# Kernel optimization log

Hardware: AMD Instinct MI355X
Metric: run time of the kernel (lower is better)

## Reference

```python
import jax, jax.numpy as jnp
import numpy as np

EPS = 1e-5
AVG_D_LOG = 2.302585092994046  # avg_d['log'] = log(10)

N, D, F, FE = 65536, 16, 64, 16
POST_IN = (4 * 3 + 1) * F  # (n_agg*n_scalers + 1) * in_dim = 832


def setup_inputs() -> dict:
    key = jax.random.key(0)
    ks = jax.random.split(key, 8)
    h = jax.random.normal(ks[0], (N, F), dtype=jnp.float32)
    edge_attr = jax.random.normal(ks[1], (N, D, FE), dtype=jnp.float32)
    nbr_idx = jax.random.randint(ks[2], (N, D), 0, N)
    pre_in = 2 * F + FE
    W_pre = jax.random.normal(ks[3], (pre_in, F), dtype=jnp.float32) / np.sqrt(pre_in)
    b_pre = jnp.zeros((F,), dtype=jnp.float32)
    W_post1 = jax.random.normal(ks[4], (POST_IN, F), dtype=jnp.float32) / np.sqrt(POST_IN)
    b_post1 = jnp.zeros((F,), dtype=jnp.float32)
    W_post2 = jax.random.normal(ks[5], (F, F), dtype=jnp.float32) / np.sqrt(F)
    b_post2 = jnp.zeros((F,), dtype=jnp.float32)
    return {"h": h, "edge_attr": edge_attr, "nbr_idx": nbr_idx,
            "W_pre": W_pre, "b_pre": b_pre,
            "W_post1": W_post1, "b_post1": b_post1,
            "W_post2": W_post2, "b_post2": b_post2}


def reference(h, edge_attr, nbr_idx, W_pre, b_pre, W_post1, b_post1, W_post2, b_post2):
    # pretrans: message MLP on cat([src_feat, dst_feat, edge_attr])
    h_src = h[nbr_idx]                                   # [N, D, F]
    h_dst = jnp.broadcast_to(h[:, None, :], h_src.shape)  # [N, D, F]
    z = jnp.concatenate([h_src, h_dst, edge_attr], axis=-1)  # [N, D, 2F+FE]
    e = jax.nn.relu(jnp.einsum('ndi,io->ndo', z, W_pre) + b_pre)  # [N, D, F]

    # multi-aggregator neighbor reduction (dim=-2)
    mean = jnp.mean(e, axis=-2)
    mx = jnp.max(e, axis=-2)
    mn = jnp.min(e, axis=-2)
    var = jax.nn.relu(jnp.mean(e * e, axis=-2) - mean * mean)
    std = jnp.sqrt(var + EPS)
    agg = jnp.concatenate([mean, mx, mn, std], axis=-1)  # [N, 4F]

    # degree scalers (fixed in-degree D)
    logD = jnp.asarray(np.log(D + 1.0), dtype=h.dtype)
    amp = agg * (logD / AVG_D_LOG)
    att = agg * (AVG_D_LOG / logD)
    agg = jnp.concatenate([agg, amp, att], axis=-1)      # [N, 12F]

    # posttrans MLP on cat([h, aggregated]) with residual (in_dim == out_dim)
    x = jnp.concatenate([h, agg], axis=-1)               # [N, 13F]
    x = jax.nn.relu(x @ W_post1 + b_post1)
    x = x @ W_post2 + b_post2
    return x + h
```

## Files before the change

### kernel.cpp

```cpp
#include <hip/hip_runtime.h>
#include <hip/hip_bf16.h>
#include <math.h>


#define N_NODES 65536
#define NBLK (N_NODES / 16)
#define GRID_PREP (NBLK + 64)
#define ASTRIDE 348
#define YSTRIDE 76

typedef float f32x4 __attribute__((ext_vector_type(4)));
typedef float f32x16 __attribute__((ext_vector_type(16)));
typedef short s16x8 __attribute__((ext_vector_type(8)));
typedef unsigned short us4 __attribute__((ext_vector_type(4)));
typedef int i32x4 __attribute__((ext_vector_type(4)));

__device__ __forceinline__ unsigned short f2bf(float f) {
    union { float f; unsigned int u; } v; v.f = f;
    unsigned int r = v.u + 0x7fffu + ((v.u >> 16) & 1u);
    return (unsigned short)(r >> 16);
}
__device__ __forceinline__ unsigned short f2bfh(float f) {
    __hip_bfloat16 b = __float2bfloat16(f);
    union { __hip_bfloat16 b; unsigned short u; } v; v.b = b; return v.u;
}
__device__ __forceinline__ float bf2f(unsigned short u) {
    union { unsigned int u; float f; } v; v.u = ((unsigned int)u) << 16; return v.f;
}

__global__ __launch_bounds__(256) void k_prep(const float* __restrict__ h,
                                              const float* __restrict__ Wpre,
                                              const float* __restrict__ b_pre,
                                              const float* __restrict__ Wp1,
                                              const float* __restrict__ Wp2,
                                              unsigned short* __restrict__ u,
                                              unsigned short* __restrict__ vbf,
                                              unsigned short* __restrict__ wfullT,
                                              unsigned short* __restrict__ w3T,
                                              unsigned short* __restrict__ wp2T,
                                              float c1, float c2) {
    int t = threadIdx.x;
    if (blockIdx.x >= NBLK) {
        int c = blockIdx.x - NBLK;
        for (int k = t; k < 320; k += 256) {
            float v;
            if (k < 64) v = Wp1[k * 64 + c];
            else {
                int kk = k - 64;
                v = Wp1[(64 + kk) * 64 + c] + c1 * Wp1[(320 + kk) * 64 + c]
                                            + c2 * Wp1[(576 + kk) * 64 + c];
            }
            wfullT[c * 320 + k] = f2bf(v);
        }
        if (t < 16)              w3T[c * 16 + t]         = f2bf(Wpre[(128 + t) * 64 + c]);
        if (t >= 64 && t < 128)  wp2T[c * 64 + (t - 64)] = f2bf(Wp2[(t - 64) * 64 + c]);
        return;
    }

    __shared__ unsigned short hl[16 * 68];
    int lane = t & 63;
    int wv = __builtin_amdgcn_readfirstlane(t) >> 6;
    int c = lane & 15, g = lane >> 4;
    int node0 = blockIdx.x * 16;
    {
        int r = t >> 4, q = t & 15;
        float4 hv = *((const float4*)(h + (size_t)node0 * 64) + t);
        us4 o;
        o.x = f2bfh(hv.x); o.y = f2bfh(hv.y); o.z = f2bfh(hv.z); o.w = f2bfh(hv.w);
        *(us4*)&hl[r * 68 + q * 4] = o;
    }
    s16x8 bf[2][2];
    int woff = (wv < 2) ? 0 : 64;
    #pragma unroll
    for (int i2 = 0; i2 < 2; ++i2) {
        int wcol = ((wv & 1) * 32) + i2 * 16 + c;
        #pragma unroll
        for (int ks = 0; ks < 2; ++ks) {
            #pragma unroll
            for (int j = 0; j < 8; ++j)
                bf[i2][ks][j] = (short)f2bfh(Wpre[(woff + ks * 32 + g * 8 + j) * 64 + wcol]);
        }
    }
    __syncthreads();
    f32x4 acc0 = {0.f, 0.f, 0.f, 0.f}, acc1 = {0.f, 0.f, 0.f, 0.f};
    #pragma unroll
    for (int ks = 0; ks < 2; ++ks) {
        s16x8 a = *(const s16x8*)&hl[c * 68 + ks * 32 + g * 8];
        acc0 = __builtin_amdgcn_mfma_f32_16x16x32_bf16(a, bf[0][ks], acc0, 0, 0, 0);
        acc1 = __builtin_amdgcn_mfma_f32_16x16x32_bf16(a, bf[1][ks], acc1, 0, 0, 0);
    }
    unsigned short* dst = (wv < 2) ? u : vbf;
    #pragma unroll
    for (int i2 = 0; i2 < 2; ++i2) {
        int dcol = ((wv & 1) * 32) + i2 * 16 + c;
        float bp = (wv < 2) ? b_pre[dcol] : 0.f;
        const f32x4& av = i2 ? acc1 : acc0;
        #pragma unroll
        for (int i = 0; i < 4; ++i) {
            int row = g * 4 + i;
            dst[(size_t)(node0 + row) * 64 + dcol] = f2bfh(av[i] + bp);
        }
    }
}

__global__ __launch_bounds__(256, 4) void k_main(
    const float* __restrict__ h,
    const float* __restrict__ edge_attr,
    const int* __restrict__ nbr_idx,
    const float* __restrict__ b_post1,
    const float* __restrict__ b_post2,
    const unsigned short* __restrict__ u,
    const unsigned short* __restrict__ vbf,
    const unsigned short* __restrict__ wfullT,
    const unsigned short* __restrict__ w3T,
    const unsigned short* __restrict__ wp2T,
    float* __restrict__ out) {
    __shared__ unsigned short A_lds[16 * ASTRIDE];
    __shared__ unsigned short y1_lds[16 * YSTRIDE];

    int t = threadIdx.x;
    int lane = t & 63;
    int wu2 = __builtin_amdgcn_readfirstlane(t) >> 6;
    int c = lane & 15;
    int g = lane >> 4;
    int l32 = lane & 31;
    int h2 = lane >> 5;
    int ct = wu2 & 1;
    int wr = wu2 >> 1;
    int colb = ct * 32 + l32;
    int cb2 = colb * 2;
    int col16 = wu2 * 16 + c;
    int node0 = blockIdx.x * 16;

    s16x8 w3b = *(const s16x8*)&w3T[colb * 16 + h2 * 8];
    float b1c = b_post1[col16];
    float b2c = b_post2[col16];

    const char* ub = (const char*)u;
    const char* vb = (const char*)vbf + ((unsigned)node0 << 7) + (unsigned)(wr * 256) + cb2;
    const char* eb = (const char*)edge_attr
                   + ((size_t)node0 * 16 + wr * 32 + l32) * 64 + h2 * 32;

    {
        int r = t >> 4, q = t & 15;
        float4 hv = *((const float4*)(h + (size_t)node0 * 64) + t);
        us4 o;
        o.x = f2bfh(hv.x); o.y = f2bfh(hv.y); o.z = f2bfh(hv.z); o.w = f2bfh(hv.w);
        *(us4*)&A_lds[r * ASTRIDE + q * 4] = o;
    }

#define ISSUE(S, IT)                                                           \
    const int* nb##S = nbr_idx + node0 * 16 + (wr + 2 * (IT)) * 32 + 4 * h2;   \
    i32x4 ja##S = *(const i32x4*)(nb##S);                                      \
    i32x4 jb##S = *(const i32x4*)(nb##S + 8);                                  \
    i32x4 jc##S = *(const i32x4*)(nb##S + 16);                                 \
    i32x4 jd##S = *(const i32x4*)(nb##S + 24);                                 \
    float4 xa##S = *(const float4*)(eb + (IT) * 4096);                         \
    float4 xb##S = *(const float4*)(eb + (IT) * 4096 + 16);                    \
    unsigned short g0##S  = *(const unsigned short*)(ub + (unsigned)((ja##S[0] << 7) + cb2)); \
    unsigned short g1##S  = *(const unsigned short*)(ub + (unsigned)((ja##S[1] << 7) + cb2)); \
    unsigned short g2##S  = *(const unsigned short*)(ub + (unsigned)((ja##S[2] << 7) + cb2)); \
    unsigned short g3##S  = *(const unsigned short*)(ub + (unsigned)((ja##S[3] << 7) + cb2)); \
    unsigned short g4##S  = *(const unsigned short*)(ub + (unsigned)((jb##S[0] << 7) + cb2)); \
    unsigned short g5##S  = *(const unsigned short*)(ub + (unsigned)((jb##S[1] << 7) + cb2)); \
    unsigned short g6##S  = *(const unsigned short*)(ub + (unsigned)((jb##S[2] << 7) + cb2)); \
    unsigned short g7##S  = *(const unsigned short*)(ub + (unsigned)((jb##S[3] << 7) + cb2)); \
    unsigned short g8##S  = *(const unsigned short*)(ub + (unsigned)((jc##S[0] << 7) + cb2)); \
    unsigned short g9##S  = *(const unsigned short*)(ub + (unsigned)((jc##S[1] << 7) + cb2)); \
    unsigned short g10##S = *(const unsigned short*)(ub + (unsigned)((jc##S[2] << 7) + cb2)); \
    unsigned short g11##S = *(const unsigned short*)(ub + (unsigned)((jc##S[3] << 7) + cb2)); \
    unsigned short g12##S = *(const unsigned short*)(ub + (unsigned)((jd##S[0] << 7) + cb2)); \
    unsigned short g13##S = *(const unsigned short*)(ub + (unsigned)((jd##S[1] << 7) + cb2)); \
    unsigned short g14##S = *(const unsigned short*)(ub + (unsigned)((jd##S[2] << 7) + cb2)); \
    unsigned short g15##S = *(const unsigned short*)(ub + (unsigned)((jd##S[3] << 7) + cb2)); \
    unsigned short va##S = *(const unsigned short*)(vb + (IT) * 512);          \
    unsigned short vc##S = *(const unsigned short*)(vb + (IT) * 512 + 128);

#define COMPUTE(S, IT) {                                                       \
    s16x8 a;                                                                   \
    a[0] = (short)f2bfh(xa##S.x); a[1] = (short)f2bfh(xa##S.y);                \
    a[2] = (short)f2bfh(xa##S.z); a[3] = (short)f2bfh(xa##S.w);                \
    a[4] = (short)f2bfh(xb##S.x); a[5] = (short)f2bfh(xb##S.y);                \
    a[6] = (short)f2bfh(xb##S.z); a[7] = (short)f2bfh(xb##S.w);                \
    f32x16 acc = {};                                                           \
    acc = __builtin_amdgcn_mfma_f32_32x32x16_bf16(a, w3b, acc, 0, 0, 0);       \
    float v0 = bf2f(va##S), v1 = bf2f(vc##S);                                  \
    float e0  = fmaxf(acc[0]  + bf2f(g0##S)  + v0, 0.f);                       \
    float e1  = fmaxf(acc[1]  + bf2f(g1##S)  + v0, 0.f);                       \
    float e2  = fmaxf(acc[2]  + bf2f(g2##S)  + v0, 0.f);                       \
    float e3  = fmaxf(acc[3]  + bf2f(g3##S)  + v0, 0.f);                       \
    float e4  = fmaxf(acc[4]  + bf2f(g4##S)  + v0, 0.f);                       \
    float e5  = fmaxf(acc[5]  + bf2f(g5##S)  + v0, 0.f);                       \
    float e6  = fmaxf(acc[6]  + bf2f(g6##S)  + v0, 0.f);                       \
    float e7  = fmaxf(acc[7]  + bf2f(g7##S)  + v0, 0.f);                       \
    float e8  = fmaxf(acc[8]  + bf2f(g8##S)  + v1, 0.f);                       \
    float e9  = fmaxf(acc[9]  + bf2f(g9##S)  + v1, 0.f);                       \
    float e10 = fmaxf(acc[10] + bf2f(g10##S) + v1, 0.f);                       \
    float e11 = fmaxf(acc[11] + bf2f(g11##S) + v1, 0.f);                       \
    float e12 = fmaxf(acc[12] + bf2f(g12##S) + v1, 0.f);                       \
    float e13 = fmaxf(acc[13] + bf2f(g13##S) + v1, 0.f);                       \
    float e14 = fmaxf(acc[14] + bf2f(g14##S) + v1, 0.f);                       \
    float e15 = fmaxf(acc[15] + bf2f(g15##S) + v1, 0.f);                       \
    float s1a = ((e0 + e1) + (e2 + e3)) + ((e4 + e5) + (e6 + e7));             \
    float s2a = fmaf(e0, e0, fmaf(e1, e1, fmaf(e2, e2, e3 * e3)))              \
              + fmaf(e4, e4, fmaf(e5, e5, fmaf(e6, e6, e7 * e7)));             \
    float mxa = fmaxf(fmaxf(fmaxf(e0, e1), fmaxf(e2, e3)),                     \
                      fmaxf(fmaxf(e4, e5), fmaxf(e6, e7)));                    \
    float mna = fminf(fminf(fminf(e0, e1), fminf(e2, e3)),                     \
                      fminf(fminf(e4, e5), fminf(e6, e7)));                    \
    float s1b = ((e8 + e9) + (e10 + e11)) + ((e12 + e13) + (e14 + e15));       \
    float s2b = fmaf(e8, e8, fmaf(e9, e9, fmaf(e10, e10, e11 * e11)))          \
              + fmaf(e12, e12, fmaf(e13, e13, fmaf(e14, e14, e15 * e15)));     \
    float mxb = fmaxf(fmaxf(fmaxf(e8, e9), fmaxf(e10, e11)),                   \
                      fmaxf(fmaxf(e12, e13), fmaxf(e14, e15)));                \
    float mnb = fminf(fminf(fminf(e8, e9), fminf(e10, e11)),                   \
                      fminf(fminf(e12, e13), fminf(e14, e15)));                \
    s1a += __shfl_xor(s1a, 32); s2a += __shfl_xor(s2a, 32);                    \
    mxa = fmaxf(mxa, __shfl_xor(mxa, 32)); mna = fminf(mna, __shfl_xor(mna, 32)); \
    s1b += __shfl_xor(s1b, 32); s2b += __shfl_xor(s2b, 32);                    \
    mxb = fmaxf(mxb, __shfl_xor(mxb, 32)); mnb = fminf(mnb, __shfl_xor(mnb, 32)); \
    float S1 = h2 ? s1b : s1a;                                                 \
    float S2 = h2 ? s2b : s2a;                                                 \
    float MX = h2 ? mxb : mxa;                                                 \
    float MN = h2 ? mnb : mna;                                                 \
    float M  = S1 * 0.0625f;                                                   \
    float SD = sqrtf(fmaxf(fmaf(-M, M, S2 * 0.0625f), 0.f) + 1e-5f);           \
    unsigned short* pd = &A_lds[(2 * (wr + 2 * (IT)) + h2) * ASTRIDE + 64 + colb]; \
    pd[0]   = f2bfh(M);                                                        \
    pd[64]  = f2bfh(MX);                                                       \
    pd[128] = f2bfh(MN);                                                       \
    pd[192] = f2bfh(SD);                                                       \
}

    ISSUE(T0, 0)
    ISSUE(T1, 1)
    COMPUTE(T0, 0)
    ISSUE(T2, 2)
    COMPUTE(T1, 1)
    ISSUE(T3, 3)
    COMPUTE(T2, 2)
    COMPUTE(T3, 3)
#undef ISSUE
#undef COMPUTE

    s16x8 wf[10];
    #pragma unroll
    for (int ks = 0; ks < 10; ++ks)
        wf[ks] = *(const s16x8*)&wfullT[col16 * 320 + ks * 32 + g * 8];
    __syncthreads();

    {
        f32x4 y1 = {0.f, 0.f, 0.f, 0.f};
        #pragma unroll
        for (int ks = 0; ks < 10; ++ks) {
            s16x8 a = *(const s16x8*)&A_lds[c * ASTRIDE + ks * 32 + g * 8];
            y1 = __builtin_amdgcn_mfma_f32_16x16x32_bf16(a, wf[ks], y1, 0, 0, 0);
        }
        #pragma unroll
        for (int i = 0; i < 4; ++i)
            y1_lds[(g * 4 + i) * YSTRIDE + col16] = f2bfh(fmaxf(y1[i] + b1c, 0.f));
    }

    s16x8 wp0 = *(const s16x8*)&wp2T[col16 * 64 + 0 * 32 + g * 8];
    s16x8 wp1 = *(const s16x8*)&wp2T[col16 * 64 + 1 * 32 + g * 8];
    __syncthreads();

    {
        f32x4 o = {0.f, 0.f, 0.f, 0.f};
        {
            s16x8 a0 = *(const s16x8*)&y1_lds[c * YSTRIDE + 0 * 32 + g * 8];
            s16x8 a1 = *(const s16x8*)&y1_lds[c * YSTRIDE + 1 * 32 + g * 8];
            o = __builtin_amdgcn_mfma_f32_16x16x32_bf16(a0, wp0, o, 0, 0, 0);
            o = __builtin_amdgcn_mfma_f32_16x16x32_bf16(a1, wp1, o, 0, 0, 0);
        }
        #pragma unroll
        for (int i = 0; i < 4; ++i) {
            int r = g * 4 + i;
            out[(size_t)(node0 + r) * 64 + col16] =
                o[i] + b2c + h[(size_t)(node0 + r) * 64 + col16];
        }
    }
}

extern "C" void kernel_launch(void* const* d_in, const int* in_sizes, int n_in,
                              void* d_out, int out_size, void* d_ws, size_t ws_size,
                              hipStream_t stream) {
    const float* h         = (const float*)d_in[0];
    const float* edge_attr = (const float*)d_in[1];
    const int*   nbr_idx   = (const int*)d_in[2];
    const float* W_pre     = (const float*)d_in[3];
    const float* b_pre     = (const float*)d_in[4];
    const float* W_post1   = (const float*)d_in[5];
    const float* b_post1   = (const float*)d_in[6];
    const float* W_post2   = (const float*)d_in[7];
    const float* b_post2   = (const float*)d_in[8];
    float* out = (float*)d_out;

    size_t need = (size_t)N_NODES * 64 * 2 * 2 + (64 * 320 + 64 * 16 + 64 * 64) * 2;
    if (ws_size < need) return;
    unsigned short* u      = (unsigned short*)d_ws;
    unsigned short* vbf    = u + (size_t)N_NODES * 64;
    unsigned short* wfullT = vbf + (size_t)N_NODES * 64;
    unsigned short* w3T    = wfullT + 64 * 320;
    unsigned short* wp2T   = w3T + 64 * 16;

    double ld = log(16.0 + 1.0);
    const double AVG = 2.302585092994046;
    float c1 = (float)(ld / AVG);
    float c2 = (float)(AVG / ld);

    k_prep<<<GRID_PREP, 256, 0, stream>>>(h, W_pre, b_pre, W_post1, W_post2,
                                          u, vbf, wfullT, w3T, wp2T, c1, c2);
    k_main<<<NBLK, 256, 0, stream>>>(h, edge_attr, nbr_idx, b_post1, b_post2,
                                     u, vbf, wfullT, w3T, wp2T, out);
}
```

Measured before the change: 66.19 us.

## Stage gathered neighbor rows in LDS with vectorized 16-byte loads

Each neighbor's bf16 u row is now gathered cooperatively as whole 128-byte rows with 16-byte vector loads into a padded LDS buffer. Before, each lane issued scattered 2-byte global loads per neighbor, one per feature column. This should cut the number of memory transactions for the gather. The cost is about 36KB of extra LDS per block, a barrier before compute, and loss of the previous issue/compute software pipelining, so occupancy is lowered to 3 blocks per CU.

```diff
diff --git a/kernel.cpp b/kernel.cpp
--- a/kernel.cpp
+++ b/kernel.cpp
@@ -6,6 +6,7 @@
 #define N_NODES 65536
 #define NBLK (N_NODES / 16)
 #define GRID_PREP (NBLK + 64)
+#define USTRIDE 72
 #define ASTRIDE 348
 #define YSTRIDE 76
 
@@ -13,7 +14,6 @@
 typedef float f32x16 __attribute__((ext_vector_type(16)));
 typedef short s16x8 __attribute__((ext_vector_type(8)));
 typedef unsigned short us4 __attribute__((ext_vector_type(4)));
-typedef int i32x4 __attribute__((ext_vector_type(4)));
 
 __device__ __forceinline__ unsigned short f2bf(float f) {
     union { float f; unsigned int u; } v; v.f = f;
@@ -103,7 +103,7 @@
     }
 }
 
-__global__ __launch_bounds__(256, 4) void k_main(
+__global__ __launch_bounds__(256, 3) void k_main(
     const float* __restrict__ h,
     const float* __restrict__ edge_attr,
     const int* __restrict__ nbr_idx,
@@ -115,6 +115,7 @@
     const unsigned short* __restrict__ w3T,
     const unsigned short* __restrict__ wp2T,
     float* __restrict__ out) {
+    __shared__ unsigned short u_lds[256 * USTRIDE];
     __shared__ unsigned short A_lds[16 * ASTRIDE];
     __shared__ unsigned short y1_lds[16 * YSTRIDE];
 
@@ -128,7 +129,6 @@
     int ct = wu2 & 1;
     int wr = wu2 >> 1;
     int colb = ct * 32 + l32;
-    int cb2 = colb * 2;
     int col16 = wu2 * 16 + c;
     int node0 = blockIdx.x * 16;
 
@@ -136,10 +136,14 @@
     float b1c = b_post1[col16];
     float b2c = b_post2[col16];
 
-    const char* ub = (const char*)u;
-    const char* vb = (const char*)vbf + ((unsigned)node0 << 7) + (unsigned)(wr * 256) + cb2;
-    const char* eb = (const char*)edge_attr
-                   + ((size_t)node0 * 16 + wr * 32 + l32) * 64 + h2 * 32;
+    #pragma unroll
+    for (int i = 0; i < 8; ++i) {
+        int row = (t >> 3) + 32 * i;
+        int chunk = t & 7;
+        int j = nbr_idx[node0 * 16 + row];
+        s16x8 d = *(const s16x8*)(u + ((size_t)j << 6) + chunk * 8);
+        *(s16x8*)&u_lds[row * USTRIDE + chunk * 8] = d;
+    }
 
     {
         int r = t >> 4, q = t & 15;
@@ -149,58 +153,61 @@
         *(us4*)&A_lds[r * ASTRIDE + q * 4] = o;
     }
 
-#define ISSUE(S, IT)                                                           \
-    const int* nb##S = nbr_idx + node0 * 16 + (wr + 2 * (IT)) * 32 + 4 * h2;   \
-    i32x4 ja##S = *(const i32x4*)(nb##S);                                      \
-    i32x4 jb##S = *(const i32x4*)(nb##S + 8);                                  \
-    i32x4 jc##S = *(const i32x4*)(nb##S + 16);                                 \
-    i32x4 jd##S = *(const i32x4*)(nb##S + 24);                                 \
-    float4 xa##S = *(const float4*)(eb + (IT) * 4096);                         \
-    float4 xb##S = *(const float4*)(eb + (IT) * 4096 + 16);                    \
-    unsigned short g0##S  = *(const unsigned short*)(ub + (unsigned)((ja##S[0] << 7) + cb2)); \
-    unsigned short g1##S  = *(const unsigned short*)(ub + (unsigned)((ja##S[1] << 7) + cb2)); \
-    unsigned short g2##S  = *(const unsigned short*)(ub + (unsigned)((ja##S[2] << 7) + cb2)); \
-    unsigned short g3##S  = *(const unsigned short*)(ub + (unsigned)((ja##S[3] << 7) + cb2)); \
-    unsigned short g4##S  = *(const unsigned short*)(ub + (unsigned)((jb##S[0] << 7) + cb2)); \
-    unsigned short g5##S  = *(const unsigned short*)(ub + (unsigned)((jb##S[1] << 7) + cb2)); \
-    unsigned short g6##S  = *(const unsigned short*)(ub + (unsigned)((jb##S[2] << 7) + cb2)); \
-    unsigned short g7##S  = *(const unsigned short*)(ub + (unsigned)((jb##S[3] << 7) + cb2)); \
-    unsigned short g8##S  = *(const unsigned short*)(ub + (unsigned)((jc##S[0] << 7) + cb2)); \
-    unsigned short g9##S  = *(const unsigned short*)(ub + (unsigned)((jc##S[1] << 7) + cb2)); \
-    unsigned short g10##S = *(const unsigned short*)(ub + (unsigned)((jc##S[2] << 7) + cb2)); \
-    unsigned short g11##S = *(const unsigned short*)(ub + (unsigned)((jc##S[3] << 7) + cb2)); \
-    unsigned short g12##S = *(const unsigned short*)(ub + (unsigned)((jd##S[0] << 7) + cb2)); \
-    unsigned short g13##S = *(const unsigned short*)(ub + (unsigned)((jd##S[1] << 7) + cb2)); \
-    unsigned short g14##S = *(const unsigned short*)(ub + (unsigned)((jd##S[2] << 7) + cb2)); \
-    unsigned short g15##S = *(const unsigned short*)(ub + (unsigned)((jd##S[3] << 7) + cb2)); \
-    unsigned short va##S = *(const unsigned short*)(vb + (IT) * 512);          \
-    unsigned short vc##S = *(const unsigned short*)(vb + (IT) * 512 + 128);
-
-#define COMPUTE(S, IT) {                                                       \
+    const char* eb = (const char*)edge_attr
+                   + ((size_t)node0 * 16 + wr * 32 + l32) * 64 + h2 * 32;
+    float4 xa0 = *(const float4*)(eb);
+    float4 xb0 = *(const float4*)(eb + 16);
+    float4 xa1 = *(const float4*)(eb + 4096);
+    float4 xb1 = *(const float4*)(eb + 4096 + 16);
+    float4 xa2 = *(const float4*)(eb + 8192);
+    float4 xb2 = *(const float4*)(eb + 8192 + 16);
+    float4 xa3 = *(const float4*)(eb + 12288);
+    float4 xb3 = *(const float4*)(eb + 12288 + 16);
+    const unsigned short* vrow = vbf + (size_t)node0 * 64;
+    unsigned short vl0 = vrow[(2 * (wr + 0)) * 64 + colb];
+    unsigned short vh0 = vrow[(2 * (wr + 0) + 1) * 64 + colb];
+    unsigned short vl1 = vrow[(2 * (wr + 2)) * 64 + colb];
+    unsigned short vh1 = vrow[(2 * (wr + 2) + 1) * 64 + colb];
+    unsigned short vl2 = vrow[(2 * (wr + 4)) * 64 + colb];
+    unsigned short vh2 = vrow[(2 * (wr + 4) + 1) * 64 + colb];
+    unsigned short vl3 = vrow[(2 * (wr + 6)) * 64 + colb];
+    unsigned short vh3 = vrow[(2 * (wr + 6) + 1) * 64 + colb];
+    __syncthreads();
+
+#define TILEC(X0, X1, VLO, VHI, RT) {                                          \
     s16x8 a;                                                                   \
-    a[0] = (short)f2bfh(xa##S.x); a[1] = (short)f2bfh(xa##S.y);                \
-    a[2] = (short)f2bfh(xa##S.z); a[3] = (short)f2bfh(xa##S.w);                \
-    a[4] = (short)f2bfh(xb##S.x); a[5] = (short)f2bfh(xb##S.y);                \
-    a[6] = (short)f2bfh(xb##S.z); a[7] = (short)f2bfh(xb##S.w);                \
+    a[0] = (short)f2bfh(X0.x); a[1] = (short)f2bfh(X0.y);                      \
+    a[2] = (short)f2bfh(X0.z); a[3] = (short)f2bfh(X0.w);                      \
+    a[4] = (short)f2bfh(X1.x); a[5] = (short)f2bfh(X1.y);                      \
+    a[6] = (short)f2bfh(X1.z); a[7] = (short)f2bfh(X1.w);                      \
     f32x16 acc = {};                                                           \
     acc = __builtin_amdgcn_mfma_f32_32x32x16_bf16(a, w3b, acc, 0, 0, 0);       \
-    float v0 = bf2f(va##S), v1 = bf2f(vc##S);                                  \
-    float e0  = fmaxf(acc[0]  + bf2f(g0##S)  + v0, 0.f);                       \
-    float e1  = fmaxf(acc[1]  + bf2f(g1##S)  + v0, 0.f);                       \
-    float e2  = fmaxf(acc[2]  + bf2f(g2##S)  + v0, 0.f);                       \
-    float e3  = fmaxf(acc[3]  + bf2f(g3##S)  + v0, 0.f);                       \
-    float e4  = fmaxf(acc[4]  + bf2f(g4##S)  + v0, 0.f);                       \
-    float e5  = fmaxf(acc[5]  + bf2f(g5##S)  + v0, 0.f);                       \
-    float e6  = fmaxf(acc[6]  + bf2f(g6##S)  + v0, 0.f);                       \
-    float e7  = fmaxf(acc[7]  + bf2f(g7##S)  + v0, 0.f);                       \
-    float e8  = fmaxf(acc[8]  + bf2f(g8##S)  + v1, 0.f);                       \
-    float e9  = fmaxf(acc[9]  + bf2f(g9##S)  + v1, 0.f);                       \
-    float e10 = fmaxf(acc[10] + bf2f(g10##S) + v1, 0.f);                       \
-    float e11 = fmaxf(acc[11] + bf2f(g11##S) + v1, 0.f);                       \
-    float e12 = fmaxf(acc[12] + bf2f(g12##S) + v1, 0.f);                       \
-    float e13 = fmaxf(acc[13] + bf2f(g13##S) + v1, 0.f);                       \
-    float e14 = fmaxf(acc[14] + bf2f(g14##S) + v1, 0.f);                       \
-    float e15 = fmaxf(acc[15] + bf2f(g15##S) + v1, 0.f);                       \
+    float uv[16];                                                              \
+    _Pragma("unroll")                                                          \
+    for (int q = 0; q < 4; ++q) {                                              \
+        int row = (RT) * 32 + 8 * q + 4 * h2;                                  \
+        uv[4 * q + 0] = bf2f(u_lds[(row + 0) * USTRIDE + colb]);               \
+        uv[4 * q + 1] = bf2f(u_lds[(row + 1) * USTRIDE + colb]);               \
+        uv[4 * q + 2] = bf2f(u_lds[(row + 2) * USTRIDE + colb]);               \
+        uv[4 * q + 3] = bf2f(u_lds[(row + 3) * USTRIDE + colb]);               \
+    }                                                                          \
+    float v0 = bf2f(VLO), v1 = bf2f(VHI);                                      \
+    float e0  = fmaxf(acc[0]  + uv[0]  + v0, 0.f);                             \
+    float e1  = fmaxf(acc[1]  + uv[1]  + v0, 0.f);                             \
+    float e2  = fmaxf(acc[2]  + uv[2]  + v0, 0.f);                             \
+    float e3  = fmaxf(acc[3]  + uv[3]  + v0, 0.f);                             \
+    float e4  = fmaxf(acc[4]  + uv[4]  + v0, 0.f);                             \
+    float e5  = fmaxf(acc[5]  + uv[5]  + v0, 0.f);                             \
+    float e6  = fmaxf(acc[6]  + uv[6]  + v0, 0.f);                             \
+    float e7  = fmaxf(acc[7]  + uv[7]  + v0, 0.f);                             \
+    float e8  = fmaxf(acc[8]  + uv[8]  + v1, 0.f);                             \
+    float e9  = fmaxf(acc[9]  + uv[9]  + v1, 0.f);                             \
+    float e10 = fmaxf(acc[10] + uv[10] + v1, 0.f);                             \
+    float e11 = fmaxf(acc[11] + uv[11] + v1, 0.f);                             \
+    float e12 = fmaxf(acc[12] + uv[12] + v1, 0.f);                             \
+    float e13 = fmaxf(acc[13] + uv[13] + v1, 0.f);                             \
+    float e14 = fmaxf(acc[14] + uv[14] + v1, 0.f);                             \
+    float e15 = fmaxf(acc[15] + uv[15] + v1, 0.f);                             \
     float s1a = ((e0 + e1) + (e2 + e3)) + ((e4 + e5) + (e6 + e7));             \
     float s2a = fmaf(e0, e0, fmaf(e1, e1, fmaf(e2, e2, e3 * e3)))              \
               + fmaf(e4, e4, fmaf(e5, e5, fmaf(e6, e6, e7 * e7)));             \
@@ -225,23 +232,18 @@
     float MN = h2 ? mnb : mna;                                                 \
     float M  = S1 * 0.0625f;                                                   \
     float SD = sqrtf(fmaxf(fmaf(-M, M, S2 * 0.0625f), 0.f) + 1e-5f);           \
-    unsigned short* pd = &A_lds[(2 * (wr + 2 * (IT)) + h2) * ASTRIDE + 64 + colb]; \
+    unsigned short* pd = &A_lds[(2 * (RT) + h2) * ASTRIDE + 64 + colb];        \
     pd[0]   = f2bfh(M);                                                        \
     pd[64]  = f2bfh(MX);                                                       \
     pd[128] = f2bfh(MN);                                                       \
     pd[192] = f2bfh(SD);                                                       \
 }
 
-    ISSUE(T0, 0)
-    ISSUE(T1, 1)
-    COMPUTE(T0, 0)
-    ISSUE(T2, 2)
-    COMPUTE(T1, 1)
-    ISSUE(T3, 3)
-    COMPUTE(T2, 2)
-    COMPUTE(T3, 3)
-#undef ISSUE
-#undef COMPUTE
+    TILEC(xa0, xb0, vl0, vh0, wr)
+    TILEC(xa1, xb1, vl1, vh1, wr + 2)
+    TILEC(xa2, xb2, vl2, vh2, wr + 4)
+    TILEC(xa3, xb3, vl3, vh3, wr + 6)
+#undef TILEC
 
     s16x8 wf[10];
     #pragma unroll
@@ -267,12 +269,10 @@
 
     {
         f32x4 o = {0.f, 0.f, 0.f, 0.f};
-        {
-            s16x8 a0 = *(const s16x8*)&y1_lds[c * YSTRIDE + 0 * 32 + g * 8];
-            s16x8 a1 = *(const s16x8*)&y1_lds[c * YSTRIDE + 1 * 32 + g * 8];
-            o = __builtin_amdgcn_mfma_f32_16x16x32_bf16(a0, wp0, o, 0, 0, 0);
-            o = __builtin_amdgcn_mfma_f32_16x16x32_bf16(a1, wp1, o, 0, 0, 0);
-        }
+        s16x8 a0 = *(const s16x8*)&y1_lds[c * YSTRIDE + 0 * 32 + g * 8];
+        s16x8 a1 = *(const s16x8*)&y1_lds[c * YSTRIDE + 1 * 32 + g * 8];
+        o = __builtin_amdgcn_mfma_f32_16x16x32_bf16(a0, wp0, o, 0, 0, 0);
+        o = __builtin_amdgcn_mfma_f32_16x16x32_bf16(a1, wp1, o, 0, 0, 0);
         #pragma unroll
         for (int i = 0; i < 4; ++i) {
             int r = g * 4 + i;
```

Result: no change. 65.35 us (-1.3%).
